# Kernel tuning notes

Measured on AMD Instinct MI355X. Metric: run time of the kernel, lower is better.

The kernel has to match this reference:

```python
import jax, jax.numpy as jnp
import numpy as np

NUM_HEADS = 8
OUT_FEATURES = 64
ALPHA = 0.2


def setup_inputs() -> dict:
    key = jax.random.key(0)
    k1, k2, k3, k4 = jax.random.split(key, 4)
    B, N, E, F_IN = 2, 8192, 4096, 256
    x = jax.random.normal(k1, (B, N, F_IN), dtype=jnp.float32)
    H = jax.random.uniform(k2, (N, E), dtype=jnp.float32)
    # xavier-like scaled params
    W = jax.random.normal(k3, (F_IN, OUT_FEATURES * NUM_HEADS), dtype=jnp.float32) * 0.05
    a_vertices = jax.random.normal(k4, (OUT_FEATURES, 1), dtype=jnp.float32) * 0.1
    return {"x": x, "H": H, "W": W, "a_vertices": a_vertices}


def reference(x, H, W, a_vertices):
    B, N, _ = x.shape
    # Wh: (B, N, heads, out)
    Wh = jnp.matmul(x, W).reshape(B, N, NUM_HEADS, OUT_FEATURES)
    # per-node, per-head attention logit: (B, N, heads)
    av = jax.nn.leaky_relu(jnp.einsum('bnhd,d->bnh', Wh, a_vertices[:, 0]), ALPHA)
    # edge attention: softmax over edges (torch dim=0 of (E, heads))
    ae = jax.nn.softmax(jnp.einsum('ne,bnh->beh', H, av), axis=1)  # (B, E, heads)
    # aggregate node features onto edges: (B, E, heads, out)
    m = jnp.einsum('ne,bnhd->behd', H, Wh)
    # scatter back to nodes with edge-attention weighting: (B, N, heads, out)
    out = jnp.einsum('ne,beh,behd->bnhd', H, ae, m)
    return out.reshape(B, N, NUM_HEADS * OUT_FEATURES)
```

## Files before the change

kernel.cpp:

```cpp
#include <hip/hip_runtime.h>

#define N_NODES 8192
#define N_EDGES 4096
#define F_INS   256
#define HEADS   8
#define DOUT    64
#define HDIM    512
#define CCOMB   1024
#define BATCH   2

typedef __bf16 bf16x8 __attribute__((ext_vector_type(8)));
typedef __bf16 bf16x4 __attribute__((ext_vector_type(4)));
typedef float  f32x4  __attribute__((ext_vector_type(4)));

__device__ __forceinline__ void gld_lds16(const __bf16* g, __bf16* l) {
    __builtin_amdgcn_global_load_lds(
        (const __attribute__((address_space(1))) void*)g,
        (__attribute__((address_space(3))) void*)l, 16, 0, 0);
}

__launch_bounds__(256, 4)
__global__ void convert_H_logits_kernel(const float* __restrict__ H,
                                        const float* __restrict__ av,
                                        __bf16* __restrict__ Hb,
                                        __bf16* __restrict__ HbT,
                                        float* __restrict__ plog) {
    __shared__ __align__(16) char smem[33280];
    float* lav = (float*)smem;
    __bf16 (*tile)[32][132] = (__bf16(*)[32][132])(smem + 16384);
    float* red = (float*)smem;

    int t = threadIdx.x;
    int e0 = blockIdx.x * 128;
    int n0 = blockIdx.y * 256;
    int equad = t & 31, r0 = t >> 5;
    int lane = t & 63, wv = t >> 6;

    for (int p = t; p < 4096; p += 256) {
        int n = p >> 4, q = p & 15, b = q >> 3, h = q & 7;
        lav[p] = av[(size_t)b * (N_NODES * 8) + (size_t)(n0 + n) * 8 + h];
    }

    const float* hbase = H + (size_t)n0 * N_EDGES + e0 + equad * 4;
    __bf16* hb_base = Hb + (size_t)n0 * N_EDGES + e0 + equad * 4;

    f32x4 acc[4][4] = {};

    __syncthreads();

    float4 v[4];
    for (int g = 0; g < 8; ++g) {
        int nb = g * 32;
#pragma unroll
        for (int k = 0; k < 4; ++k) {
            int n = nb + r0 + 8 * k;
            v[k] = *(const float4*)(hbase + (size_t)n * N_EDGES);
        }
        if (g > 0) {
            int pb = (g - 1) & 1, pnb = (g - 1) * 32;
#pragma unroll
            for (int s = 0; s < 2; ++s) {
                int id = s * 256 + t;
                int er = id >> 2, oct = id & 3;
                bf16x8 val;
#pragma unroll
                for (int j = 0; j < 8; ++j) val[j] = tile[pb][oct * 8 + j][er];
                *(bf16x8*)(HbT + (size_t)(e0 + er) * N_NODES + n0 + pnb + oct * 8) = val;
            }
        }
        int buf = g & 1;
#pragma unroll
        for (int k = 0; k < 4; ++k) {
            int n = nb + r0 + 8 * k;
            const f32x4* lrow = (const f32x4*)&lav[n * 16];
            float4 vv = v[k];
#pragma unroll
            for (int qq = 0; qq < 4; ++qq) {
                f32x4 l = lrow[qq];
                acc[0][qq] += l * vv.x;
                acc[1][qq] += l * vv.y;
                acc[2][qq] += l * vv.z;
                acc[3][qq] += l * vv.w;
            }
            bf16x4 hb;
            hb.x = (__bf16)vv.x; hb.y = (__bf16)vv.y;
            hb.z = (__bf16)vv.z; hb.w = (__bf16)vv.w;
            *(bf16x4*)(hb_base + (size_t)n * N_EDGES) = hb;
            *(bf16x4*)&tile[buf][r0 + 8 * k][equad * 4] = hb;
        }
        __syncthreads();
    }
    {
        int pnb = 7 * 32;
#pragma unroll
        for (int s = 0; s < 2; ++s) {
            int id = s * 256 + t;
            int er = id >> 2, oct = id & 3;
            bf16x8 val;
#pragma unroll
            for (int j = 0; j < 8; ++j) val[j] = tile[1][oct * 8 + j][er];
            *(bf16x8*)(HbT + (size_t)(e0 + er) * N_NODES + n0 + pnb + oct * 8) = val;
        }
    }

#pragma unroll
    for (int ec = 0; ec < 4; ++ec)
#pragma unroll
        for (int qq = 0; qq < 4; ++qq)
#pragma unroll
            for (int qi = 0; qi < 4; ++qi)
                acc[ec][qq][qi] += __shfl_xor(acc[ec][qq][qi], 32, 64);

    __syncthreads();
    if (lane < 32) {
#pragma unroll
        for (int qq = 0; qq < 4; ++qq)
#pragma unroll
            for (int qi = 0; qi < 4; ++qi) {
                f32x4 tmp = {acc[0][qq][qi], acc[1][qq][qi],
                             acc[2][qq][qi], acc[3][qq][qi]};
                *(f32x4*)&red[wv * 2048 + (qq * 4 + qi) * 128 + equad * 4] = tmp;
            }
    }
    __syncthreads();
#pragma unroll
    for (int s = 0; s < 8; ++s) {
        int id = s * 256 + t;
        int q = id >> 7, el = id & 127;
        float sum = red[q * 128 + el] + red[2048 + q * 128 + el] +
                    red[4096 + q * 128 + el] + red[6144 + q * 128 + el];
        plog[((size_t)blockIdx.y * 16 + q) * N_EDGES + e0 + el] = sum;
    }
}

__launch_bounds__(256)
__global__ void reduce_logits_kernel(const float* __restrict__ plog,
                                     float* __restrict__ logits) {
    int id = blockIdx.x * 256 + threadIdx.x;
    int q = id >> 12, e = id & 4095;
    float s = 0.f;
#pragma unroll
    for (int nb = 0; nb < 32; ++nb)
        s += plog[((size_t)nb * 16 + q) * N_EDGES + e];
    logits[(size_t)q * N_EDGES + e] = s;
}

__launch_bounds__(256)
__global__ void wbt_kernel(const float* __restrict__ W, __bf16* __restrict__ WbT) {
    int i = blockIdx.x * 256 + threadIdx.x;
    int c = i >> 8, f = i & 255;
    WbT[i] = (__bf16)W[(size_t)f * HDIM + c];
}

__launch_bounds__(256)
__global__ void wa_kernel(const float* __restrict__ W, const float* __restrict__ a,
                          float* __restrict__ Wa) {
    int i = blockIdx.x * 256 + threadIdx.x;
    if (i >= F_INS * HEADS) return;
    int f = i >> 3, h = i & 7;
    float s = 0.f;
#pragma unroll 8
    for (int d = 0; d < DOUT; ++d) s += W[(size_t)f * HDIM + h * DOUT + d] * a[d];
    Wa[i] = s;
}

__launch_bounds__(256)
__global__ void av_kernel(const float* __restrict__ x, const float* __restrict__ Wa,
                          float* __restrict__ av, __bf16* __restrict__ xb) {
    __shared__ float lx[32][257];
    __shared__ float lwa[F_INS * HEADS];
    int t = threadIdx.x;
    size_t row0 = (size_t)blockIdx.x * 32;
    for (int p = t; p < F_INS * HEADS; p += 256) lwa[p] = Wa[p];
#pragma unroll
    for (int p = 0; p < 32; ++p) {
        float v = x[(row0 + p) * F_INS + t];
        lx[p][t] = v;
        xb[(row0 + p) * F_INS + t] = (__bf16)v;
    }
    __syncthreads();
    int r = t >> 3, h = t & 7;
    float acc = 0.f;
#pragma unroll 8
    for (int f = 0; f < F_INS; ++f) acc += lx[r][f] * lwa[f * 8 + h];
    av[(row0 + r) * 8 + h] = acc > 0.f ? acc : 0.2f * acc;
}

__launch_bounds__(256)
__global__ void softmax_kernel(float* __restrict__ logits) {
    __shared__ float red[4];
    __shared__ float reds[4];
    int t = threadIdx.x;
    float* row = logits + (size_t)blockIdx.x * N_EDGES;
    float mx = -1e30f;
    for (int i = t; i < N_EDGES; i += 256) mx = fmaxf(mx, row[i]);
#pragma unroll
    for (int o = 32; o > 0; o >>= 1) mx = fmaxf(mx, __shfl_xor(mx, o, 64));
    if ((t & 63) == 0) red[t >> 6] = mx;
    __syncthreads();
    mx = fmaxf(fmaxf(red[0], red[1]), fmaxf(red[2], red[3]));
    float s = 0.f;
    for (int i = t; i < N_EDGES; i += 256) {
        float v = expf(row[i] - mx);
        row[i] = v;
        s += v;
    }
#pragma unroll
    for (int o = 32; o > 0; o >>= 1) s += __shfl_xor(s, o, 64);
    if ((t & 63) == 0) reds[t >> 6] = s;
    __syncthreads();
    float inv = 1.0f / (reds[0] + reds[1] + reds[2] + reds[3]);
    for (int i = t; i < N_EDGES; i += 256) row[i] *= inv;
}

template <int MODE>
__launch_bounds__(256, 4)
__global__ void gemm_bt(const __bf16* __restrict__ A, const __bf16* __restrict__ BT,
                        int lda, int ldbt, int K,
                        size_t a_bz, size_t bt_bz, size_t out_z,
                        __bf16* __restrict__ outB, int ldo,
                        float* __restrict__ outF) {
    __shared__ __bf16 AsF[8192];
    __shared__ __bf16 BsF[8192];
    int t = threadIdx.x;
    int bz = blockIdx.z;
    A  += (size_t)bz * a_bz;
    BT += (size_t)bz * bt_bz;
    if (MODE == 0) outB += (size_t)bz * out_z;
    if (MODE == 1) outF += (size_t)bz * out_z;
    size_t m0 = (size_t)blockIdx.y * 128;
    size_t n0 = (size_t)blockIdx.x * 128;

    int lane = t & 63, wv = t >> 6;
    int ln = lane & 15, lk = lane >> 4;

    const __bf16* pA[4]; const __bf16* pB[4];
    __bf16* lA[4]; __bf16* lB[4];
#pragma unroll
    for (int p = 0; p < 4; ++p) {
        int bid = wv * 4 + p;
        int mb = bid >> 1, kb = bid & 1;
        pA[p] = A + (m0 + mb * 16 + ln) * (size_t)lda + kb * 32 + lk * 8;
        pB[p] = BT + (n0 + mb * 16 + ln) * (size_t)ldbt + kb * 32 + lk * 8;
        lA[p] = &AsF[bid * 512];
        lB[p] = &BsF[bid * 512];
    }

    int wm16 = (wv & 1) * 4, wn16 = (wv >> 1) * 4;
    f32x4 acc[4][4] = {};

    for (int k0 = 0; k0 < K; k0 += 64) {
        __syncthreads();
#pragma unroll
        for (int p = 0; p < 4; ++p) gld_lds16(pA[p] + k0, lA[p]);
#pragma unroll
        for (int p = 0; p < 4; ++p) gld_lds16(pB[p] + k0, lB[p]);
        __syncthreads();
#pragma unroll
        for (int ksb = 0; ksb < 2; ++ksb) {
            bf16x8 af[4], bfr[4];
#pragma unroll
            for (int i = 0; i < 4; ++i)
                af[i] = *(const bf16x8*)&AsF[((wm16 + i) * 2 + ksb) * 512 + lane * 8];
#pragma unroll
            for (int j = 0; j < 4; ++j)
                bfr[j] = *(const bf16x8*)&BsF[((wn16 + j) * 2 + ksb) * 512 + lane * 8];
#pragma unroll
            for (int i = 0; i < 4; ++i)
#pragma unroll
                for (int j = 0; j < 4; ++j)
                    acc[i][j] = __builtin_amdgcn_mfma_f32_16x16x32_bf16(
                        af[i], bfr[j], acc[i][j], 0, 0, 0);
        }
    }

    int wm = (wv & 1) * 64, wn = (wv >> 1) * 64;
#pragma unroll
    for (int i = 0; i < 4; ++i)
#pragma unroll
        for (int j = 0; j < 4; ++j)
#pragma unroll
            for (int rg = 0; rg < 4; ++rg) {
                int gm = (int)m0 + wm + i * 16 + lk * 4 + rg;
                int gc = (int)n0 + wn + j * 16 + ln;
                float v = acc[i][j][rg];
                if (MODE == 0) {
                    outB[(size_t)gm * ldo + gc] = (__bf16)v;
                } else if (MODE == 1) {
                    outF[(size_t)gm * ldo + gc] = v;
                } else {
                    outF[(size_t)(gc >> 9) * ((size_t)N_NODES * HDIM) +
                         (size_t)gm * HDIM + (gc & 511)] = v;
                }
            }
}

template <int SWZ>
__launch_bounds__(512, 2)
__global__ void gemm256(const __bf16* __restrict__ A, const __bf16* __restrict__ BT,
                        int lda, int ldbt, int K,
                        size_t a_bz, size_t bt_bz, size_t out_z,
                        float* __restrict__ outF, int ldo) {
    __shared__ __bf16 lds[2 * 2 * 32 * 512];
#define LOFF(b, op, fr) ((((b) * 2 + (op)) * 32 + (fr)) * 512)
    int bx, by, bz;
    if (SWZ) {
        int g = (int)blockIdx.x + 4 * ((int)blockIdx.y + 32 * (int)blockIdx.z);
        int xcd = g & 7, j = g >> 3;
        int l = (j & 3) + 4 * xcd + 32 * (j >> 2);
        bx = l & 3; by = (l >> 2) & 31; bz = l >> 7;
    } else {
        bx = blockIdx.x; by = blockIdx.y; bz = blockIdx.z;
    }
    A    += (size_t)bz * a_bz;
    BT   += (size_t)bz * bt_bz;
    outF += (size_t)bz * out_z;
    size_t m0 = (size_t)by * 256;
    size_t n0 = (size_t)bx * 256;

    int t = threadIdx.x;
    int lane = t & 63, wv = t >> 6;
    int ln = lane & 15, lk = lane >> 4;
    int wmf = (wv >> 2) * 8;
    int wnf = (wv & 3) * 4;

    int mbA0 = (wv < 4) ? wv : wv + 4;
    int mbA1 = (wv < 4) ? wv + 4 : wv + 8;
    int nbB0 = (wv >> 1) * 4 + (wv & 1);
    int nbB1 = nbB0 + 2;
    const __bf16* gA0 = A + (m0 + mbA0 * 16 + ln) * (size_t)lda + lk * 8;
    const __bf16* gA1 = A + (m0 + mbA1 * 16 + ln) * (size_t)lda + lk * 8;
    const __bf16* gB0 = BT + (n0 + nbB0 * 16 + ln) * (size_t)ldbt + lk * 8;
    const __bf16* gB1 = BT + (n0 + nbB1 * 16 + ln) * (size_t)ldbt + lk * 8;

    int NT = K >> 6;

    gld_lds16(gA0, &lds[LOFF(0, 0, mbA0 * 2 + 0)]);
    gld_lds16(gA0 + 32, &lds[LOFF(0, 0, mbA0 * 2 + 1)]);
    gld_lds16(gB0, &lds[LOFF(0, 1, nbB0 * 2 + 0)]);
    gld_lds16(gB0 + 32, &lds[LOFF(0, 1, nbB0 * 2 + 1)]);
    gld_lds16(gB1, &lds[LOFF(0, 1, nbB1 * 2 + 0)]);
    gld_lds16(gB1 + 32, &lds[LOFF(0, 1, nbB1 * 2 + 1)]);
    gld_lds16(gA1, &lds[LOFF(0, 0, mbA1 * 2 + 0)]);
    gld_lds16(gA1 + 32, &lds[LOFF(0, 0, mbA1 * 2 + 1)]);
    asm volatile("s_waitcnt vmcnt(4)" ::: "memory");
    __builtin_amdgcn_s_barrier();
    __builtin_amdgcn_sched_barrier(0);

    f32x4 acc[8][4] = {};

#define PHASE(TL, P, DO_STAGE, VMN)                                            \
    {                                                                          \
        const int c_ = (TL) & 1;                                               \
        bf16x8 af_[4][2], bf_[2][2];                                           \
        _Pragma("unroll") for (int mi = 0; mi < 4; ++mi)                       \
            _Pragma("unroll") for (int ks = 0; ks < 2; ++ks)                   \
                af_[mi][ks] = *(const bf16x8*)&lds[                            \
                    LOFF(c_, 0, (wmf + ((P) >> 1) * 4 + mi) * 2 + ks) + lane * 8]; \
        _Pragma("unroll") for (int nj = 0; nj < 2; ++nj)                       \
            _Pragma("unroll") for (int ks = 0; ks < 2; ++ks)                   \
                bf_[nj][ks] = *(const bf16x8*)&lds[                            \
                    LOFF(c_, 1, (wnf + ((P) & 1) * 2 + nj) * 2 + ks) + lane * 8]; \
        if (DO_STAGE) {                                                        \
            const int ub_ = ((TL) + 1) & 1;                                    \
            const int ko_ = ((TL) + 1) * 64;                                   \
            if ((P) == 0) {                                                    \
                gld_lds16(gA0 + ko_, &lds[LOFF(ub_, 0, mbA0 * 2 + 0)]);        \
                gld_lds16(gA0 + ko_ + 32, &lds[LOFF(ub_, 0, mbA0 * 2 + 1)]);   \
            } else if ((P) == 1) {                                             \
                gld_lds16(gB0 + ko_, &lds[LOFF(ub_, 1, nbB0 * 2 + 0)]);        \
                gld_lds16(gB0 + ko_ + 32, &lds[LOFF(ub_, 1, nbB0 * 2 + 1)]);   \
            } else if ((P) == 2) {                                             \
                gld_lds16(gB1 + ko_, &lds[LOFF(ub_, 1, nbB1 * 2 + 0)]);        \
                gld_lds16(gB1 + ko_ + 32, &lds[LOFF(ub_, 1, nbB1 * 2 + 1)]);   \
            } else {                                                           \
                gld_lds16(gA1 + ko_, &lds[LOFF(ub_, 0, mbA1 * 2 + 0)]);        \
                gld_lds16(gA1 + ko_ + 32, &lds[LOFF(ub_, 0, mbA1 * 2 + 1)]);   \
            }                                                                  \
        }                                                                      \
        if ((VMN) >= 0)                                                        \
            asm volatile("s_waitcnt vmcnt(%0)" ::"i"(VMN) : "memory");         \
        __builtin_amdgcn_s_barrier();                                          \
        __builtin_amdgcn_sched_barrier(0);                                     \
        __builtin_amdgcn_s_setprio(1);                                         \
        _Pragma("unroll") for (int mi = 0; mi < 4; ++mi)                       \
            _Pragma("unroll") for (int nj = 0; nj < 2; ++nj)                   \
                _Pragma("unroll") for (int ks = 0; ks < 2; ++ks)               \
                    acc[((P) >> 1) * 4 + mi][((P) & 1) * 2 + nj] =             \
                        __builtin_amdgcn_mfma_f32_16x16x32_bf16(               \
                            af_[mi][ks], bf_[nj][ks],                          \
                            acc[((P) >> 1) * 4 + mi][((P) & 1) * 2 + nj],      \
                            0, 0, 0);                                          \
        __builtin_amdgcn_s_setprio(0);                                         \
    }

    for (int tl = 0; tl < NT - 1; ++tl) {
        PHASE(tl, 0, 1, 4);
        PHASE(tl, 1, 1, 4);
        PHASE(tl, 2, 1, 4);
        PHASE(tl, 3, 1, 4);
    }
    PHASE(NT - 1, 0, 0, 2);
    PHASE(NT - 1, 1, 0, 0);
    PHASE(NT - 1, 2, 0, -1);
    PHASE(NT - 1, 3, 0, -1);
#undef PHASE
#undef LOFF

    int wm = (wv >> 2) * 128, wn = (wv & 3) * 64;
#pragma unroll
    for (int i = 0; i < 8; ++i)
#pragma unroll
        for (int j = 0; j < 4; ++j)
#pragma unroll
            for (int rg = 0; rg < 4; ++rg) {
                int gm = (int)m0 + wm + i * 16 + lk * 4 + rg;
                int gc = (int)n0 + wn + j * 16 + ln;
                outF[(size_t)gm * ldo + gc] = acc[i][j][rg];
            }
}

__launch_bounds__(256)
__global__ void scale1_kernel(const float* __restrict__ acc1, const float* __restrict__ ae,
                              __bf16* __restrict__ mwT) {
    int i = blockIdx.x * 256 + threadIdx.x;
    size_t base = (size_t)i * 4;
    int c = (int)(base >> 12);
    int e = (int)(base & 4095);
    const size_t slab = (size_t)CCOMB * N_EDGES / 4;
    float4 s0 = ((const float4*)acc1)[i];
    float4 s1 = ((const float4*)acc1)[i + slab];
    float4 s2 = ((const float4*)acc1)[i + 2 * slab];
    float4 s3 = ((const float4*)acc1)[i + 3 * slab];
    float4 a4 = *(const float4*)(ae + ((size_t)(c >> 6) << 12) + e);
    bf16x4 o;
    o.x = (__bf16)((s0.x + s1.x + s2.x + s3.x) * a4.x);
    o.y = (__bf16)((s0.y + s1.y + s2.y + s3.y) * a4.y);
    o.z = (__bf16)((s0.z + s1.z + s2.z + s3.z) * a4.z);
    o.w = (__bf16)((s0.w + s1.w + s2.w + s3.w) * a4.w);
    ((bf16x4*)mwT)[i] = o;
}

__launch_bounds__(256)
__global__ void reduce2_kernel(const float* __restrict__ s, float* __restrict__ out) {
    int i = blockIdx.x * 256 + threadIdx.x;
    size_t base = (size_t)i * 4;
    int m = (int)(base >> 10);
    int c = (int)(base & 1023);
    const size_t slab = (size_t)N_NODES * CCOMB / 4;
    float4 a = ((const float4*)s)[i];
    float4 b = ((const float4*)s)[i + slab];
    float4 o;
    o.x = a.x + b.x; o.y = a.y + b.y; o.z = a.z + b.z; o.w = a.w + b.w;
    *(float4*)&out[(size_t)(c >> 9) * ((size_t)N_NODES * HDIM) +
                   (size_t)m * HDIM + (c & 511)] = o;
}

extern "C" void kernel_launch(void* const* d_in, const int* in_sizes, int n_in,
                              void* d_out, int out_size, void* d_ws, size_t ws_size,
                              hipStream_t stream) {
    const float* x = (const float*)d_in[0];
    const float* H = (const float*)d_in[1];
    const float* W = (const float*)d_in[2];
    const float* a = (const float*)d_in[3];
    float* out = (float*)d_out;

    char* p = (char*)d_ws;
    __bf16* Hb   = (__bf16*)p; p += (size_t)N_NODES * N_EDGES * 2;
    __bf16* HbT  = (__bf16*)p; p += (size_t)N_EDGES * N_NODES * 2;
    __bf16* xb   = (__bf16*)p; p += (size_t)BATCH * N_NODES * F_INS * 2;
    __bf16* WbT  = (__bf16*)p; p += (size_t)HDIM * F_INS * 2;
    __bf16* WhbT = (__bf16*)p; p += (size_t)CCOMB * N_NODES * 2;
    __bf16* mwT  = (__bf16*)p; p += (size_t)CCOMB * N_EDGES * 2;
    float*  Wa   = (float*)p;  p += (size_t)F_INS * HEADS * 4;
    float*  av   = (float*)p;  p += (size_t)BATCH * N_NODES * HEADS * 4;
    float*  ae   = (float*)p;  p += (size_t)16 * N_EDGES * 4;
    float*  acc1 = (float*)p;  p += (size_t)4 * CCOMB * N_EDGES * 4;
    float*  plog = acc1;

    wbt_kernel<<<dim3(HDIM * F_INS / 256), 256, 0, stream>>>(W, WbT);
    wa_kernel<<<dim3(8), 256, 0, stream>>>(W, a, Wa);
    av_kernel<<<dim3(BATCH * N_NODES / 32), 256, 0, stream>>>(x, Wa, av, xb);
    convert_H_logits_kernel<<<dim3(N_EDGES / 128, N_NODES / 256), 256, 0, stream>>>(
        H, av, Hb, HbT, plog);
    reduce_logits_kernel<<<dim3(256), 256, 0, stream>>>(plog, ae);
    softmax_kernel<<<dim3(16), 256, 0, stream>>>(ae);

    gemm_bt<0><<<dim3(64, 4, 2), 256, 0, stream>>>(
        WbT, xb, F_INS, F_INS, F_INS,
        0, (size_t)N_NODES * F_INS, (size_t)HDIM * N_NODES,
        WhbT, N_NODES, nullptr);

    gemm256<0><<<dim3(16, 4, 4), 512, 0, stream>>>(
        WhbT, HbT, N_NODES, N_NODES, 2048,
        2048, 2048, (size_t)CCOMB * N_EDGES,
        acc1, N_EDGES);

    scale1_kernel<<<dim3(CCOMB * N_EDGES / 4 / 256), 256, 0, stream>>>(acc1, ae, mwT);

    gemm256<1><<<dim3(4, 32, 2), 512, 0, stream>>>(
        Hb, mwT, N_EDGES, N_EDGES, 2048,
        2048, 2048, (size_t)N_NODES * CCOMB,
        acc1, CCOMB);

    reduce2_kernel<<<dim3(N_NODES * CCOMB / 4 / 256), 256, 0, stream>>>(acc1, out);
}
```

Before: 476.0 us.

## Stage H tiles into LDS with async global-to-LDS loads and swizzle GEMM blocks

The H conversion kernel now loads fp32 H tiles straight into a double-buffered LDS region with global_load_lds and manual vmcnt waits. Both the bf16 row-major and transposed outputs are produced from LDS, replacing the register prefetch and separate bf16 transpose tile. The first big GEMM also gets an XCD-aware block remapping so blocks that share a panel run on the same chiplet for better L2 reuse. The cost is more LDS per block, with occupancy lowered to 3, and hand-tuned waitcnt logic that could be fragile.

Result: no change. 474.7 us (-0.3%).

```diff
diff --git a/kernel.cpp b/kernel.cpp
--- a/kernel.cpp
+++ b/kernel.cpp
@@ -19,89 +19,95 @@
         (__attribute__((address_space(3))) void*)l, 16, 0, 0);
 }
 
-__launch_bounds__(256, 4)
+__launch_bounds__(256, 3)
 __global__ void convert_H_logits_kernel(const float* __restrict__ H,
                                         const float* __restrict__ av,
                                         __bf16* __restrict__ Hb,
                                         __bf16* __restrict__ HbT,
                                         float* __restrict__ plog) {
-    __shared__ __align__(16) char smem[33280];
-    float* lav = (float*)smem;
-    __bf16 (*tile)[32][132] = (__bf16(*)[32][132])(smem + 16384);
-    float* red = (float*)smem;
+    __shared__ __align__(16) float smem[12288];
+    float* lav  = smem;
+    float* hbuf = smem + 4096;
+    float* red  = hbuf;
 
     int t = threadIdx.x;
     int e0 = blockIdx.x * 128;
     int n0 = blockIdx.y * 256;
+    int lane = t & 63, wv = t >> 6;
     int equad = t & 31, r0 = t >> 5;
-    int lane = t & 63, wv = t >> 6;
 
     for (int p = t; p < 4096; p += 256) {
         int n = p >> 4, q = p & 15, b = q >> 3, h = q & 7;
         lav[p] = av[(size_t)b * (N_NODES * 8) + (size_t)(n0 + n) * 8 + h];
     }
 
-    const float* hbase = H + (size_t)n0 * N_EDGES + e0 + equad * 4;
-    __bf16* hb_base = Hb + (size_t)n0 * N_EDGES + e0 + equad * 4;
+    const float* gsrc = H + (size_t)(n0 + 8 * wv + (lane >> 5)) * N_EDGES
+                          + e0 + (lane & 31) * 4;
+
+#define STAGE_H(GG, BUF)                                                        \
+    {                                                                           \
+        _Pragma("unroll")                                                       \
+        for (int c = 0; c < 4; ++c)                                             \
+            gld_lds16((const __bf16*)(gsrc + ((size_t)(GG) * 32 + 2 * c) * N_EDGES), \
+                      (__bf16*)(hbuf + (BUF) * 4096 + (8 * wv + 2 * c) * 128)); \
+    }
+
+    STAGE_H(0, 0);
+    STAGE_H(1, 1);
+    asm volatile("s_waitcnt vmcnt(4) lgkmcnt(0)" ::: "memory");
+    __builtin_amdgcn_s_barrier();
+    __builtin_amdgcn_sched_barrier(0);
 
     f32x4 acc[4][4] = {};
 
-    __syncthreads();
-
-    float4 v[4];
     for (int g = 0; g < 8; ++g) {
-        int nb = g * 32;
+        int cb = g & 1;
+        const float* hb = hbuf + cb * 4096;
 #pragma unroll
         for (int k = 0; k < 4; ++k) {
-            int n = nb + r0 + 8 * k;
-            v[k] = *(const float4*)(hbase + (size_t)n * N_EDGES);
-        }
-        if (g > 0) {
-            int pb = (g - 1) & 1, pnb = (g - 1) * 32;
-#pragma unroll
-            for (int s = 0; s < 2; ++s) {
-                int id = s * 256 + t;
-                int er = id >> 2, oct = id & 3;
-                bf16x8 val;
-#pragma unroll
-                for (int j = 0; j < 8; ++j) val[j] = tile[pb][oct * 8 + j][er];
-                *(bf16x8*)(HbT + (size_t)(e0 + er) * N_NODES + n0 + pnb + oct * 8) = val;
-            }
-        }
-        int buf = g & 1;
-#pragma unroll
-        for (int k = 0; k < 4; ++k) {
-            int n = nb + r0 + 8 * k;
+            int r = r0 + 8 * k;
+            int n = g * 32 + r;
+            f32x4 vv = *(const f32x4*)(hb + r * 128 + equad * 4);
             const f32x4* lrow = (const f32x4*)&lav[n * 16];
-            float4 vv = v[k];
 #pragma unroll
             for (int qq = 0; qq < 4; ++qq) {
                 f32x4 l = lrow[qq];
-                acc[0][qq] += l * vv.x;
-                acc[1][qq] += l * vv.y;
-                acc[2][qq] += l * vv.z;
-                acc[3][qq] += l * vv.w;
+                acc[0][qq] += l * vv[0];
+                acc[1][qq] += l * vv[1];
+                acc[2][qq] += l * vv[2];
+                acc[3][qq] += l * vv[3];
             }
-            bf16x4 hb;
-            hb.x = (__bf16)vv.x; hb.y = (__bf16)vv.y;
-            hb.z = (__bf16)vv.z; hb.w = (__bf16)vv.w;
-            *(bf16x4*)(hb_base + (size_t)n * N_EDGES) = hb;
-            *(bf16x4*)&tile[buf][r0 + 8 * k][equad * 4] = hb;
+            bf16x4 hbv;
+            hbv[0] = (__bf16)vv[0]; hbv[1] = (__bf16)vv[1];
+            hbv[2] = (__bf16)vv[2]; hbv[3] = (__bf16)vv[3];
+            *(bf16x4*)(Hb + (size_t)(n0 + n) * N_EDGES + e0 + equad * 4) = hbv;
         }
-        __syncthreads();
-    }
-    {
-        int pnb = 7 * 32;
-#pragma unroll
-        for (int s = 0; s < 2; ++s) {
-            int id = s * 256 + t;
-            int er = id >> 2, oct = id & 3;
-            bf16x8 val;
-#pragma unroll
-            for (int j = 0; j < 8; ++j) val[j] = tile[1][oct * 8 + j][er];
-            *(bf16x8*)(HbT + (size_t)(e0 + er) * N_NODES + n0 + pnb + oct * 8) = val;
+        {
+            int er = t >> 1, half = t & 1;
+            const float* colp = hb + half * 16 * 128 + er;
+            bf16x8 v0, v1;
+#pragma unroll
+            for (int j = 0; j < 8; ++j) v0[j] = (__bf16)colp[j * 128];
+#pragma unroll
+            for (int j = 0; j < 8; ++j) v1[j] = (__bf16)colp[(8 + j) * 128];
+            __bf16* dst = HbT + (size_t)(e0 + er) * N_NODES + n0 + g * 32 + half * 16;
+            *(bf16x8*)dst = v0;
+            *(bf16x8*)(dst + 8) = v1;
         }
-    }
+        asm volatile("s_waitcnt lgkmcnt(0)" ::: "memory");
+        __builtin_amdgcn_s_barrier();
+        __builtin_amdgcn_sched_barrier(0);
+        if (g < 6) STAGE_H(g + 2, cb);
+        if (g < 7) {
+            if (g == 6)
+                asm volatile("s_waitcnt vmcnt(6)" ::: "memory");
+            else
+                asm volatile("s_waitcnt vmcnt(10)" ::: "memory");
+            __builtin_amdgcn_s_barrier();
+            __builtin_amdgcn_sched_barrier(0);
+        }
+    }
+#undef STAGE_H
 
 #pragma unroll
     for (int ec = 0; ec < 4; ++ec)
@@ -111,7 +117,6 @@
             for (int qi = 0; qi < 4; ++qi)
                 acc[ec][qq][qi] += __shfl_xor(acc[ec][qq][qi], 32, 64);
 
-    __syncthreads();
     if (lane < 32) {
 #pragma unroll
         for (int qq = 0; qq < 4; ++qq)
@@ -304,11 +309,16 @@
     __shared__ __bf16 lds[2 * 2 * 32 * 512];
 #define LOFF(b, op, fr) ((((b) * 2 + (op)) * 32 + (fr)) * 512)
     int bx, by, bz;
-    if (SWZ) {
+    if (SWZ == 1) {
         int g = (int)blockIdx.x + 4 * ((int)blockIdx.y + 32 * (int)blockIdx.z);
         int xcd = g & 7, j = g >> 3;
         int l = (j & 3) + 4 * xcd + 32 * (j >> 2);
         bx = l & 3; by = (l >> 2) & 31; bz = l >> 7;
+    } else if (SWZ == 2) {
+        int g = (int)blockIdx.x + 16 * ((int)blockIdx.y + 4 * (int)blockIdx.z);
+        int xcd = g & 7, j = g >> 3;
+        int pan = xcd * 2 + (j >> 4);
+        bx = j & 15; by = pan & 3; bz = pan >> 2;
     } else {
         bx = blockIdx.x; by = blockIdx.y; bz = blockIdx.z;
     }
@@ -491,7 +501,7 @@
         0, (size_t)N_NODES * F_INS, (size_t)HDIM * N_NODES,
         WhbT, N_NODES, nullptr);
 
-    gemm256<0><<<dim3(16, 4, 4), 512, 0, stream>>>(
+    gemm256<2><<<dim3(16, 4, 4), 512, 0, stream>>>(
         WhbT, HbT, N_NODES, N_NODES, 2048,
         2048, 2048, (size_t)CCOMB * N_EDGES,
         acc1, N_EDGES);
```

## Split H transpose into separate kernel and swizzle first aggregation GEMM blocks by XCD

Applied to the files above, without the earlier changes.

Removes the in-kernel transposed bf16 write from the H conversion/logit kernel and adds a standalone 64x64 LDS-tiled transpose that reads Hb back to produce HbT. This lightens the conversion kernel's LDS use, syncs and strided writes, at the cost of an extra 64 MB read pass plus a kernel launch. It also adds a new block-index swizzle for the first 256-tile GEMM that groups panels per XCD to improve L2 reuse of the shared operand.

Result: faster. 461.8 us (-3.0%).

```diff
diff --git a/kernel.cpp b/kernel.cpp
--- a/kernel.cpp
+++ b/kernel.cpp
@@ -19,16 +19,14 @@
         (__attribute__((address_space(3))) void*)l, 16, 0, 0);
 }
 
-__launch_bounds__(256, 4)
-__global__ void convert_H_logits_kernel(const float* __restrict__ H,
-                                        const float* __restrict__ av,
-                                        __bf16* __restrict__ Hb,
-                                        __bf16* __restrict__ HbT,
-                                        float* __restrict__ plog) {
-    __shared__ __align__(16) char smem[33280];
-    float* lav = (float*)smem;
-    __bf16 (*tile)[32][132] = (__bf16(*)[32][132])(smem + 16384);
-    float* red = (float*)smem;
+__launch_bounds__(256)
+__global__ void convert_hb_logits_kernel(const float* __restrict__ H,
+                                         const float* __restrict__ av,
+                                         __bf16* __restrict__ Hb,
+                                         float* __restrict__ plog) {
+    __shared__ __align__(16) float smem[8192];
+    float* lav = smem;
+    float* red = smem;
 
     int t = threadIdx.x;
     int e0 = blockIdx.x * 128;
@@ -40,40 +38,19 @@
         int n = p >> 4, q = p & 15, b = q >> 3, h = q & 7;
         lav[p] = av[(size_t)b * (N_NODES * 8) + (size_t)(n0 + n) * 8 + h];
     }
+    __syncthreads();
 
     const float* hbase = H + (size_t)n0 * N_EDGES + e0 + equad * 4;
     __bf16* hb_base = Hb + (size_t)n0 * N_EDGES + e0 + equad * 4;
 
     f32x4 acc[4][4] = {};
 
-    __syncthreads();
-
-    float4 v[4];
     for (int g = 0; g < 8; ++g) {
-        int nb = g * 32;
 #pragma unroll
         for (int k = 0; k < 4; ++k) {
-            int n = nb + r0 + 8 * k;
-            v[k] = *(const float4*)(hbase + (size_t)n * N_EDGES);
-        }
-        if (g > 0) {
-            int pb = (g - 1) & 1, pnb = (g - 1) * 32;
-#pragma unroll
-            for (int s = 0; s < 2; ++s) {
-                int id = s * 256 + t;
-                int er = id >> 2, oct = id & 3;
-                bf16x8 val;
-#pragma unroll
-                for (int j = 0; j < 8; ++j) val[j] = tile[pb][oct * 8 + j][er];
-                *(bf16x8*)(HbT + (size_t)(e0 + er) * N_NODES + n0 + pnb + oct * 8) = val;
-            }
-        }
-        int buf = g & 1;
-#pragma unroll
-        for (int k = 0; k < 4; ++k) {
-            int n = nb + r0 + 8 * k;
+            int n = g * 32 + r0 + 8 * k;
+            float4 vv = *(const float4*)(hbase + (size_t)n * N_EDGES);
             const f32x4* lrow = (const f32x4*)&lav[n * 16];
-            float4 vv = v[k];
 #pragma unroll
             for (int qq = 0; qq < 4; ++qq) {
                 f32x4 l = lrow[qq];
@@ -83,23 +60,9 @@
                 acc[3][qq] += l * vv.w;
             }
             bf16x4 hb;
-            hb.x = (__bf16)vv.x; hb.y = (__bf16)vv.y;
-            hb.z = (__bf16)vv.z; hb.w = (__bf16)vv.w;
+            hb[0] = (__bf16)vv.x; hb[1] = (__bf16)vv.y;
+            hb[2] = (__bf16)vv.z; hb[3] = (__bf16)vv.w;
             *(bf16x4*)(hb_base + (size_t)n * N_EDGES) = hb;
-            *(bf16x4*)&tile[buf][r0 + 8 * k][equad * 4] = hb;
-        }
-        __syncthreads();
-    }
-    {
-        int pnb = 7 * 32;
-#pragma unroll
-        for (int s = 0; s < 2; ++s) {
-            int id = s * 256 + t;
-            int er = id >> 2, oct = id & 3;
-            bf16x8 val;
-#pragma unroll
-            for (int j = 0; j < 8; ++j) val[j] = tile[1][oct * 8 + j][er];
-            *(bf16x8*)(HbT + (size_t)(e0 + er) * N_NODES + n0 + pnb + oct * 8) = val;
         }
     }
 
@@ -130,6 +93,32 @@
         float sum = red[q * 128 + el] + red[2048 + q * 128 + el] +
                     red[4096 + q * 128 + el] + red[6144 + q * 128 + el];
         plog[((size_t)blockIdx.y * 16 + q) * N_EDGES + e0 + el] = sum;
+    }
+}
+
+__launch_bounds__(256)
+__global__ void transpose_hb_kernel(const __bf16* __restrict__ Hb,
+                                    __bf16* __restrict__ HbT) {
+    __shared__ __bf16 tile[64][65];
+    int t = threadIdx.x;
+    int e0 = blockIdx.x * 64;
+    int n0 = blockIdx.y * 64;
+    int oct = t & 7, rq = t >> 3;
+#pragma unroll
+    for (int p = 0; p < 2; ++p) {
+        int rr = rq + 32 * p;
+        bf16x8 v = *(const bf16x8*)(Hb + (size_t)(n0 + rr) * N_EDGES + e0 + oct * 8);
+#pragma unroll
+        for (int j = 0; j < 8; ++j) tile[oct * 8 + j][rr] = v[j];
+    }
+    __syncthreads();
+#pragma unroll
+    for (int p = 0; p < 2; ++p) {
+        int er = rq + 32 * p;
+        bf16x8 w;
+#pragma unroll
+        for (int j = 0; j < 8; ++j) w[j] = tile[er][oct * 8 + j];
+        *(bf16x8*)(HbT + (size_t)(e0 + er) * N_NODES + n0 + oct * 8) = w;
     }
 }
 
@@ -304,11 +293,16 @@
     __shared__ __bf16 lds[2 * 2 * 32 * 512];
 #define LOFF(b, op, fr) ((((b) * 2 + (op)) * 32 + (fr)) * 512)
     int bx, by, bz;
-    if (SWZ) {
+    if (SWZ == 1) {
         int g = (int)blockIdx.x + 4 * ((int)blockIdx.y + 32 * (int)blockIdx.z);
         int xcd = g & 7, j = g >> 3;
         int l = (j & 3) + 4 * xcd + 32 * (j >> 2);
         bx = l & 3; by = (l >> 2) & 31; bz = l >> 7;
+    } else if (SWZ == 2) {
+        int g = (int)blockIdx.x + 16 * ((int)blockIdx.y + 4 * (int)blockIdx.z);
+        int xcd = g & 7, j = g >> 3;
+        int pan = xcd * 2 + (j >> 4);
+        bx = j & 15; by = pan & 3; bz = pan >> 2;
     } else {
         bx = blockIdx.x; by = blockIdx.y; bz = blockIdx.z;
     }
@@ -481,8 +475,9 @@
     wbt_kernel<<<dim3(HDIM * F_INS / 256), 256, 0, stream>>>(W, WbT);
     wa_kernel<<<dim3(8), 256, 0, stream>>>(W, a, Wa);
     av_kernel<<<dim3(BATCH * N_NODES / 32), 256, 0, stream>>>(x, Wa, av, xb);
-    convert_H_logits_kernel<<<dim3(N_EDGES / 128, N_NODES / 256), 256, 0, stream>>>(
-        H, av, Hb, HbT, plog);
+    convert_hb_logits_kernel<<<dim3(N_EDGES / 128, N_NODES / 256), 256, 0, stream>>>(
+        H, av, Hb, plog);
+    transpose_hb_kernel<<<dim3(N_EDGES / 64, N_NODES / 64), 256, 0, stream>>>(Hb, HbT);
     reduce_logits_kernel<<<dim3(256), 256, 0, stream>>>(plog, ae);
     softmax_kernel<<<dim3(16), 256, 0, stream>>>(ae);
 
@@ -491,7 +486,7 @@
         0, (size_t)N_NODES * F_INS, (size_t)HDIM * N_NODES,
         WhbT, N_NODES, nullptr);
 
-    gemm256<0><<<dim3(16, 4, 4), 512, 0, stream>>>(
+    gemm256<2><<<dim3(16, 4, 4), 512, 0, stream>>>(
         WhbT, HbT, N_NODES, N_NODES, 2048,
         2048, 2048, (size_t)CCOMB * N_EDGES,
         acc1, N_EDGES);
```
